# Kernel optimization log

Measured on AMD Instinct MI355X. Metric: run time of the kernel, lower is better.

## Reference

```python
import jax, jax.numpy as jnp
import numpy as np

L, H, E, V, BS = 12, 12, 768, 50257, 1024  # layers, heads, n_embd, vocab, block_size
B, T = 2, 1024
D = E // H


def setup_inputs() -> dict:
    key = jax.random.key(0)
    ks = jax.random.split(key, 10)
    s = 0.02
    d = {}
    d["idx"] = jax.random.randint(ks[0], (B, T), 0, V)
    d["targets"] = jax.random.randint(ks[1], (B, T), 0, V)
    # embeddings (wte tied with lm_head)
    d["wte"] = (jax.random.normal(ks[2], (V, E)) * s).astype(jnp.float32)
    d["wpe"] = (jax.random.normal(ks[3], (BS, E)) * s).astype(jnp.float32)
    # stacked per-layer params; Linear weights stored [in, out] (= torch W.T)
    d["ln1_w"] = jnp.ones((L, E), jnp.float32)
    d["ln1_b"] = jnp.zeros((L, E), jnp.float32)
    d["attn_w"] = (jax.random.normal(ks[4], (L, E, 3 * E)) * s).astype(jnp.float32)
    d["attn_b"] = jnp.zeros((L, 3 * E), jnp.float32)
    d["proj_w"] = (jax.random.normal(ks[5], (L, E, E)) * s).astype(jnp.float32)
    d["proj_b"] = jnp.zeros((L, E), jnp.float32)
    d["ln2_w"] = jnp.ones((L, E), jnp.float32)
    d["ln2_b"] = jnp.zeros((L, E), jnp.float32)
    d["fc_w"] = (jax.random.normal(ks[6], (L, E, 4 * E)) * s).astype(jnp.float32)
    d["fc_b"] = jnp.zeros((L, 4 * E), jnp.float32)
    d["fcproj_w"] = (jax.random.normal(ks[7], (L, 4 * E, E)) * s).astype(jnp.float32)
    d["fcproj_b"] = jnp.zeros((L, E), jnp.float32)
    d["lnf_w"] = jnp.ones((E,), jnp.float32)
    d["lnf_b"] = jnp.zeros((E,), jnp.float32)
    return d


def _ln(x, w, b, eps=1e-5):
    m = jnp.mean(x, -1, keepdims=True)
    v = jnp.mean(jnp.square(x - m), -1, keepdims=True)
    return (x - m) * jax.lax.rsqrt(v + eps) * w + b


def _block(x, p, mask):
    l1w, l1b, aw, ab, pw, pb, l2w, l2b, fw, fb, fpw, fpb = p
    Bx, Tx, C = x.shape
    # causal self-attention (explicit QK^T + mask + softmax + AV, as in source)
    qkv = _ln(x, l1w, l1b) @ aw + ab                       # [B,T,3E]
    q, k, v = jnp.split(qkv, 3, axis=-1)
    q = q.reshape(Bx, Tx, H, D).transpose(0, 2, 1, 3)       # [B,H,T,D]
    k = k.reshape(Bx, Tx, H, D).transpose(0, 2, 1, 3)
    v = v.reshape(Bx, Tx, H, D).transpose(0, 2, 1, 3)
    att = jnp.einsum('bhqd,bhkd->bhqk', q, k) * (1.0 / np.sqrt(D))
    att = jnp.where(mask, att, -jnp.inf)
    att = jax.nn.softmax(att, axis=-1)
    y = jnp.einsum('bhqk,bhkd->bhqd', att, v)
    y = y.transpose(0, 2, 1, 3).reshape(Bx, Tx, C)
    x = x + y @ pw + pb
    # MLP with tanh-approx GELU
    h = jax.nn.gelu(_ln(x, l2w, l2b) @ fw + fb, approximate=True)
    x = x + h @ fpw + fpb
    return x


def reference(idx, targets, wte, wpe, ln1_w, ln1_b, attn_w, attn_b, proj_w, proj_b,
              ln2_w, ln2_b, fc_w, fc_b, fcproj_w, fcproj_b, lnf_w, lnf_b):
    Tq = idx.shape[1]
    x = wte[idx] + wpe[:Tq]                                 # [B,T,E]
    mask = jnp.tril(jnp.ones((Tq, Tq), dtype=bool))

    def step(x, p):
        return _block(x, p, mask), None

    layer_params = (ln1_w, ln1_b, attn_w, attn_b, proj_w, proj_b,
                    ln2_w, ln2_b, fc_w, fc_b, fcproj_w, fcproj_b)
    x, _ = jax.lax.scan(step, x, layer_params)
    x = _ln(x, lnf_w, lnf_b)
    logits = x @ wte.T                                      # tied lm_head, [B,T,V]
    logp = jax.nn.log_softmax(logits, axis=-1)
    nll = -jnp.take_along_axis(logp, targets[..., None], axis=-1)[..., 0]
    loss = jnp.mean(nll)
    return logits, loss
```

## Files before the change

### kernel.cpp

```cpp
#include <hip/hip_runtime.h>
#include <hip/hip_bf16.h>
#include <math.h>

#define LNUM 12
#define HNUM 12
#define EDIM 768
#define VDIM 50257
#define BDIM 2
#define TDIM 1024
#define BT (BDIM*TDIM)
#define E3 (3*EDIM)
#define E4 (4*EDIM)
#define NPB (2*((VDIM+127)/128))

typedef __bf16 bf16x8 __attribute__((ext_vector_type(8)));
typedef __bf16 bf16x4 __attribute__((ext_vector_type(4)));
typedef float f32x4 __attribute__((ext_vector_type(4)));

__device__ __forceinline__ float gelu_f(float x) {
    float u = 0.7978845608028654f * (x + 0.044715f * x * x * x);
    return 0.5f * x * (1.0f + tanhf(u));
}

__device__ __forceinline__ void gl16(const void* g, void* l) {
    __builtin_amdgcn_global_load_lds(
        (const __attribute__((address_space(1))) unsigned int*)g,
        (__attribute__((address_space(3))) unsigned int*)l,
        16, 0, 0);
}

__global__ __launch_bounds__(256) void embed_kernel(
    const int* __restrict__ idx, const float* __restrict__ wte,
    const float* __restrict__ wpe, float* __restrict__ x)
{
    const int row = blockIdx.x;
    const int t = row % TDIM;
    const int tok = idx[row];
    const float* we = wte + (size_t)tok * EDIM;
    const float* pe = wpe + (size_t)t * EDIM;
    float* xr = x + (size_t)row * EDIM;
    for (int e = threadIdx.x; e < EDIM; e += 256) xr[e] = we[e] + pe[e];
}

__global__ __launch_bounds__(256) void ln_kernel(
    const float* __restrict__ in, const float* __restrict__ w,
    const float* __restrict__ b, __bf16* __restrict__ out)
{
    const int row = blockIdx.x * 4 + (threadIdx.x >> 6);
    const int lane = threadIdx.x & 63;
    const float4* xr = (const float4*)(in + (size_t)row * EDIM);
    float4 a0 = xr[lane], a1 = xr[64 + lane], a2 = xr[128 + lane];
    float s = a0.x + a0.y + a0.z + a0.w + a1.x + a1.y + a1.z + a1.w
            + a2.x + a2.y + a2.z + a2.w;
    #pragma unroll
    for (int off = 32; off; off >>= 1) s += __shfl_xor(s, off);
    const float mean = s * (1.0f / EDIM);
    float4 d0 = make_float4(a0.x - mean, a0.y - mean, a0.z - mean, a0.w - mean);
    float4 d1 = make_float4(a1.x - mean, a1.y - mean, a1.z - mean, a1.w - mean);
    float4 d2 = make_float4(a2.x - mean, a2.y - mean, a2.z - mean, a2.w - mean);
    float v = d0.x*d0.x + d0.y*d0.y + d0.z*d0.z + d0.w*d0.w
            + d1.x*d1.x + d1.y*d1.y + d1.z*d1.z + d1.w*d1.w
            + d2.x*d2.x + d2.y*d2.y + d2.z*d2.z + d2.w*d2.w;
    #pragma unroll
    for (int off = 32; off; off >>= 1) v += __shfl_xor(v, off);
    const float inv = rsqrtf(v * (1.0f / EDIM) + 1e-5f);
    const float4* w4 = (const float4*)w;
    const float4* b4 = (const float4*)b;
    __bf16* orow = out + (size_t)row * EDIM;
    #pragma unroll
    for (int c = 0; c < 3; ++c) {
        float4 dd = c == 0 ? d0 : (c == 1 ? d1 : d2);
        float4 ww = w4[c * 64 + lane], bb = b4[c * 64 + lane];
        bf16x4 o;
        o[0] = (__bf16)(dd.x * inv * ww.x + bb.x);
        o[1] = (__bf16)(dd.y * inv * ww.y + bb.y);
        o[2] = (__bf16)(dd.z * inv * ww.z + bb.z);
        o[3] = (__bf16)(dd.w * inv * ww.w + bb.w);
        *(bf16x4*)(orow + c * 256 + lane * 4) = o;
    }
}

__global__ __launch_bounds__(256) void redln_kernel(
    const float* __restrict__ ps, const float* __restrict__ bias,
    float* __restrict__ x, const float* __restrict__ w,
    const float* __restrict__ b, __bf16* __restrict__ out)
{
    const int row = blockIdx.x * 4 + (threadIdx.x >> 6);
    const int lane = threadIdx.x & 63;
    const float4* p0 = (const float4*)(ps + (size_t)row * EDIM);
    const float4* p1 = (const float4*)(ps + (size_t)(BT + row) * EDIM);
    float4* xr = (float4*)(x + (size_t)row * EDIM);
    const float4* b4 = (const float4*)bias;
    float4 a[3];
    #pragma unroll
    for (int c = 0; c < 3; ++c) {
        const int i = c * 64 + lane;
        float4 u = p0[i], v = p1[i], xx = xr[i], bb = b4[i];
        a[c] = make_float4(u.x + v.x + xx.x + bb.x, u.y + v.y + xx.y + bb.y,
                           u.z + v.z + xx.z + bb.z, u.w + v.w + xx.w + bb.w);
        xr[i] = a[c];
    }
    float s = a[0].x + a[0].y + a[0].z + a[0].w + a[1].x + a[1].y + a[1].z + a[1].w
            + a[2].x + a[2].y + a[2].z + a[2].w;
    #pragma unroll
    for (int off = 32; off; off >>= 1) s += __shfl_xor(s, off);
    const float mean = s * (1.0f / EDIM);
    float v = 0.f;
    #pragma unroll
    for (int c = 0; c < 3; ++c) {
        a[c] = make_float4(a[c].x - mean, a[c].y - mean, a[c].z - mean, a[c].w - mean);
        v += a[c].x * a[c].x + a[c].y * a[c].y + a[c].z * a[c].z + a[c].w * a[c].w;
    }
    #pragma unroll
    for (int off = 32; off; off >>= 1) v += __shfl_xor(v, off);
    const float inv = rsqrtf(v * (1.0f / EDIM) + 1e-5f);
    const float4* w4 = (const float4*)w;
    const float4* lb4 = (const float4*)b;
    __bf16* orow = out + (size_t)row * EDIM;
    #pragma unroll
    for (int c = 0; c < 3; ++c) {
        float4 ww = w4[c * 64 + lane], bb = lb4[c * 64 + lane];
        bf16x4 o;
        o[0] = (__bf16)(a[c].x * inv * ww.x + bb.x);
        o[1] = (__bf16)(a[c].y * inv * ww.y + bb.y);
        o[2] = (__bf16)(a[c].z * inv * ww.z + bb.z);
        o[3] = (__bf16)(a[c].w * inv * ww.w + bb.w);
        *(bf16x4*)(orow + c * 256 + lane * 4) = o;
    }
}

__global__ __launch_bounds__(256) void convt_kernel(
    const float* __restrict__ in, __bf16* __restrict__ out, int K, int N)
{
    in  += (size_t)blockIdx.z * K * N;
    out += (size_t)blockIdx.z * K * N;
    __shared__ float t[32][33];
    const int n0 = blockIdx.x * 32, k0 = blockIdx.y * 32;
    const int r = threadIdx.x >> 3, c = (threadIdx.x & 7) * 4;
    float4 v = *(const float4*)(in + (size_t)(k0 + r) * N + n0 + c);
    t[r][c + 0] = v.x; t[r][c + 1] = v.y; t[r][c + 2] = v.z; t[r][c + 3] = v.w;
    __syncthreads();
    bf16x4 o;
    o[0] = (__bf16)t[c + 0][r];
    o[1] = (__bf16)t[c + 1][r];
    o[2] = (__bf16)t[c + 2][r];
    o[3] = (__bf16)t[c + 3][r];
    *(bf16x4*)(out + (size_t)(n0 + r) * K + k0 + c) = o;
}

__global__ __launch_bounds__(256) void cvt_kernel(
    const float* __restrict__ in, __bf16* __restrict__ out, long n4)
{
    for (long i = blockIdx.x * 256L + threadIdx.x; i < n4; i += (long)gridDim.x * 256L) {
        float4 v = ((const float4*)in)[i];
        out[i * 4 + 0] = (__bf16)v.x;
        out[i * 4 + 1] = (__bf16)v.y;
        out[i * 4 + 2] = (__bf16)v.z;
        out[i * 4 + 3] = (__bf16)v.w;
    }
}

template<int BM, int BN, int BK, bool BIAS, bool GELU_, bool RES_, bool OUTBF, bool NGUARD>
__global__ __launch_bounds__(256, 2) void mgemm(
    const __bf16* __restrict__ A, const __bf16* __restrict__ Bt,
    const float* __restrict__ bias, const float* __restrict__ res,
    void* __restrict__ Cout, int M, int N, int K, int lda)
{
    constexpr int WM = BM / 2, WN = BN / 2;
    constexpr int FM = WM / 16, FN = WN / 16;
    constexpr int KS = BK / 32;
    constexpr int TBA = BM * BK * 2;
    constexpr int TBB = BN * BK * 2;
    constexpr int rA = TBA / 4096, rB = TBB / 4096;
    constexpr int RPI = 2048 / BK;
    constexpr int CPR = BK / 8;
    __shared__ __align__(16) __bf16 As[3 * BM * BK];
    __shared__ __align__(16) __bf16 Bs[3 * BN * BK];
    const int tid = threadIdx.x;
    const int lane = tid & 63;
    const int wave = tid >> 6;
    const int wr = wave >> 1, wc = wave & 1;

    const int bm = blockIdx.y, bn = blockIdx.x;
    const int m0 = bm * BM;
    const int n0 = bn * BN;
    const int kbase = blockIdx.z * K;
    const size_t zoff = (size_t)blockIdx.z * M * N;

    const int srow = tid / CPR;
    const int skey = (BK == 32) ? ((srow >> 1) & 3) : (srow & 7);
    const int c0 = (tid % CPR) ^ skey;

    const __bf16* gA = A + (size_t)(m0 + srow) * lda + kbase + c0 * 8;
    const __bf16* gB[rB];
    #pragma unroll
    for (int r = 0; r < rB; ++r) {
        int nr = n0 + srow + r * RPI;
        if (NGUARD) nr = nr < N ? nr : N - 1;
        gB[r] = Bt + (size_t)nr * lda + kbase + c0 * 8;
    }

    const int fr = lane & 15;
    const int g = lane >> 4;
    const int fkey = (BK == 32) ? ((fr >> 1) & 3) : (fr & 7);

    f32x4 acc[FM][FN];
    #pragma unroll
    for (int i = 0; i < FM; i++)
        #pragma unroll
        for (int j = 0; j < FN; j++) acc[i][j] = (f32x4){0.f, 0.f, 0.f, 0.f};

    const int nt = K / BK;

    auto stage = [&](int kk, int b) {
        #pragma unroll
        for (int r = 0; r < rA; ++r)
            gl16(gA + (size_t)r * RPI * lda + kk, (char*)As + b * TBA + r * 4096 + tid * 16);
        #pragma unroll
        for (int r = 0; r < rB; ++r)
            gl16(gB[r] + kk, (char*)Bs + b * TBB + r * 4096 + tid * 16);
    };

    stage(0, 0);
    if (nt > 1) stage(BK, 1);

    int b0 = 0, b1 = 1, b2 = 2;
    for (int t = 0; t < nt; ++t) {
        if (t + 1 < nt) {
            static_assert(rA + rB == 4 || rA + rB == 6, "vmcnt literal");
            if constexpr (rA + rB == 4) asm volatile("s_waitcnt vmcnt(4)" ::: "memory");
            else                        asm volatile("s_waitcnt vmcnt(6)" ::: "memory");
        } else {
            asm volatile("s_waitcnt vmcnt(0)" ::: "memory");
        }
        asm volatile("s_barrier" ::: "memory");
        if (t + 2 < nt) stage((t + 2) * BK, b2);

        const char* pa = (const char*)As + b0 * TBA;
        const char* pb = (const char*)Bs + b0 * TBB;
        bf16x8 af[FM][KS], bfr[FN][KS];
        #pragma unroll
        for (int i = 0; i < FM; i++)
            #pragma unroll
            for (int kc = 0; kc < KS; kc++)
                af[i][kc] = *(const bf16x8*)(pa + (wr * WM + i * 16 + fr) * (2 * BK)
                                                + (((kc * 4 + g) ^ fkey) << 4));
        #pragma unroll
        for (int j = 0; j < FN; j++)
            #pragma unroll
            for (int kc = 0; kc < KS; kc++)
                bfr[j][kc] = *(const bf16x8*)(pb + (wc * WN + j * 16 + fr) * (2 * BK)
                                                 + (((kc * 4 + g) ^ fkey) << 4));
        #pragma unroll
        for (int kc = 0; kc < KS; kc++)
            #pragma unroll
            for (int i = 0; i < FM; i++)
                #pragma unroll
                for (int j = 0; j < FN; j++)
                    acc[i][j] = __builtin_amdgcn_mfma_f32_16x16x32_bf16(af[i][kc], bfr[j][kc], acc[i][j], 0, 0, 0);
        const int tmp = b0; b0 = b1; b1 = b2; b2 = tmp;
    }

    const int crow = g * 4;
    #pragma unroll
    for (int i = 0; i < FM; i++) {
        #pragma unroll
        for (int r = 0; r < 4; r++) {
            const int m = m0 + wr * WM + i * 16 + crow + r;
            #pragma unroll
            for (int j = 0; j < FN; j++) {
                const int n = n0 + wc * WN + j * 16 + fr;
                if (!NGUARD || n < N) {
                    float v = acc[i][j][r];
                    if (BIAS) v += bias[n];
                    if (GELU_) v = gelu_f(v);
                    if (RES_) v += res[(size_t)m * N + n];
                    if (OUTBF) ((__bf16*)Cout)[zoff + (size_t)m * N + n] = (__bf16)v;
                    else       ((float*)Cout)[zoff + (size_t)m * N + n] = v;
                }
            }
        }
    }
}

__global__ __launch_bounds__(512, 1) void lgemm(
    const __bf16* __restrict__ A, const __bf16* __restrict__ Bt,
    float* __restrict__ Cout, float* __restrict__ part, int M, int N, int K)
{
    __shared__ __align__(16) __bf16 As[3 * 256 * 64];
    __shared__ __align__(16) __bf16 Bs[3 * 128 * 64];
    const int tid = threadIdx.x;
    const int lane = tid & 63;
    const int wave = tid >> 6;
    const int wm = wave >> 1, wn = wave & 1;

    const int wg = blockIdx.x;
    const int bm = (wg >> 3) & 7;
    const int bn = (wg & 7) + ((wg >> 6) << 3);
    if (bn * 128 >= N) return;
    const int m0 = bm * 256, n0 = bn * 128;

    const int srow = tid >> 3;
    const int c0 = (tid & 7) ^ (srow & 7);
    const __bf16* gA = A + (size_t)(m0 + srow) * K + c0 * 8;
    const __bf16* gB[2];
    #pragma unroll
    for (int r = 0; r < 2; ++r) {
        int nr = n0 + r * 64 + srow;
        nr = nr < N ? nr : N - 1;
        gB[r] = Bt + (size_t)nr * K + c0 * 8;
    }

    const int fr = lane & 15;
    const int g = lane >> 4;
    const int fk = fr & 7;

    auto stageA = [&](int kk, int b, int r) {
        gl16(gA + (size_t)r * 64 * K + kk, (char*)As + b * 32768 + r * 8192 + tid * 16);
    };
    auto stageB = [&](int kk, int b, int r) {
        gl16(gB[r] + kk, (char*)Bs + b * 16384 + r * 8192 + tid * 16);
    };

    f32x4 acc[4][4];
    #pragma unroll
    for (int i = 0; i < 4; i++)
        #pragma unroll
        for (int j = 0; j < 4; j++) acc[i][j] = (f32x4){0.f, 0.f, 0.f, 0.f};

    const int nt = K >> 6;
    #pragma unroll
    for (int r = 0; r < 4; ++r) stageA(0, 0, r);
    #pragma unroll
    for (int r = 0; r < 2; ++r) stageB(0, 0, r);
    #pragma unroll
    for (int r = 0; r < 4; ++r) stageA(64, 1, r);
    #pragma unroll
    for (int r = 0; r < 2; ++r) stageB(64, 1, r);

    for (int t = 0; t < nt; ++t) {
        const int bt = t % 3;
        if (t + 1 < nt) asm volatile("s_waitcnt vmcnt(6)" ::: "memory");
        else            asm volatile("s_waitcnt vmcnt(0)" ::: "memory");
        asm volatile("s_barrier" ::: "memory");

        const char* pa = (const char*)As + bt * 32768;
        const char* pb = (const char*)Bs + bt * 16384;
        const int kk2 = (t + 2) * 64;
        const int b2 = (t + 2) % 3;

        bf16x8 bfr[4][2], af[2][2];
        #pragma unroll
        for (int j = 0; j < 4; ++j)
            #pragma unroll
            for (int kc = 0; kc < 2; ++kc)
                bfr[j][kc] = *(const bf16x8*)(pb + (wn * 64 + j * 16 + fr) * 128
                                                 + (((kc * 4 + g) ^ fk) << 4));
        #pragma unroll
        for (int i = 0; i < 2; ++i)
            #pragma unroll
            for (int kc = 0; kc < 2; ++kc)
                af[i][kc] = *(const bf16x8*)(pa + (wm * 64 + i * 16 + fr) * 128
                                                + (((kc * 4 + g) ^ fk) << 4));
        if (t + 2 < nt) { stageA(kk2, b2, 0); stageA(kk2, b2, 1); stageA(kk2, b2, 2); }
        __builtin_amdgcn_s_setprio(1);
        #pragma unroll
        for (int kc = 0; kc < 2; ++kc)
            #pragma unroll
            for (int i = 0; i < 2; ++i)
                #pragma unroll
                for (int j = 0; j < 4; ++j)
                    acc[i][j] = __builtin_amdgcn_mfma_f32_16x16x32_bf16(af[i][kc], bfr[j][kc], acc[i][j], 0, 0, 0);
        __builtin_amdgcn_s_setprio(0);

        bf16x8 af1[2][2];
        #pragma unroll
        for (int i = 0; i < 2; ++i)
            #pragma unroll
            for (int kc = 0; kc < 2; ++kc)
                af1[i][kc] = *(const bf16x8*)(pa + (wm * 64 + (i + 2) * 16 + fr) * 128
                                                 + (((kc * 4 + g) ^ fk) << 4));
        if (t + 2 < nt) { stageA(kk2, b2, 3); stageB(kk2, b2, 0); stageB(kk2, b2, 1); }
        __builtin_amdgcn_s_setprio(1);
        #pragma unroll
        for (int kc = 0; kc < 2; ++kc)
            #pragma unroll
            for (int i = 0; i < 2; ++i)
                #pragma unroll
                for (int j = 0; j < 4; ++j)
                    acc[i + 2][j] = __builtin_amdgcn_mfma_f32_16x16x32_bf16(af1[i][kc], bfr[j][kc], acc[i + 2][j], 0, 0, 0);
        __builtin_amdgcn_s_setprio(0);
    }

    const int crow = g * 4;
    const int cg = bn * 2 + wn;
    #pragma unroll
    for (int i = 0; i < 4; i++) {
        #pragma unroll
        for (int r = 0; r < 4; r++) {
            const int m = m0 + wm * 64 + i * 16 + crow + r;
            float se = 0.f;
            #pragma unroll
            for (int j = 0; j < 4; j++) {
                const int n = n0 + wn * 64 + j * 16 + fr;
                if (n < N) {
                    float v = acc[i][j][r];
                    __builtin_nontemporal_store(v, &Cout[(size_t)m * N + n]);
                    se += __expf(v);
                }
            }
            se += __shfl_xor(se, 1); se += __shfl_xor(se, 2);
            se += __shfl_xor(se, 4); se += __shfl_xor(se, 8);
            if (fr == 0 && (n0 + wn * 64) < N)
                part[(size_t)m * NPB + cg] = se;
        }
    }
}

__global__ __launch_bounds__(128) void fattn_kernel(
    const __bf16* __restrict__ qkv, __bf16* __restrict__ y)
{
    const int bq = gridDim.x - 1 - blockIdx.x;
    const int h = blockIdx.y, b = blockIdx.z;
    const int tid = threadIdx.x, lane = tid & 63, w = tid >> 6;
    const int fr = lane & 15, g = lane >> 4;

    __shared__ __align__(16) __bf16 Ks[64 * 64];
    __shared__ __align__(16) __bf16 Vt[64 * 64];
    __shared__ __align__(16) __bf16 Ps[2][16 * 64];

    const __bf16* base = qkv + (size_t)b * TDIM * E3;
    const int q0w = bq * 32 + w * 16;
    const int NT = (bq >> 1) + 1;
    const int last = NT - 1;

    bf16x8 qf[2];
    {
        const __bf16* qp = base + (size_t)(q0w + fr) * E3 + h * 64 + g * 8;
        qf[0] = *(const bf16x8*)qp;
        qf[1] = *(const bf16x8*)(qp + 32);
        const __bf16 sc = (__bf16)0.125f;
        #pragma unroll
        for (int e = 0; e < 8; ++e) { qf[0][e] *= sc; qf[1][e] *= sc; }
    }

    const int r0 = tid >> 3, ch = tid & 7;
    bf16x8 kr[4], vr[4];

    #pragma unroll
    for (int it = 0; it < 4; ++it) {
        const int row = it * 16 + r0;
        const __bf16* gp = base + (size_t)row * E3 + EDIM + h * 64 + ch * 8;
        kr[it] = *(const bf16x8*)gp;
        vr[it] = *(const bf16x8*)(gp + EDIM);
    }
    #pragma unroll
    for (int it = 0; it < 4; ++it) {
        const int row = it * 16 + r0;
        *(bf16x8*)(Ks + row * 64 + ((ch ^ (row & 7)) << 3)) = kr[it];
        #pragma unroll
        for (int j = 0; j < 8; ++j) {
            const int d = ch * 8 + j;
            const int key = ((d >> 3) ^ d) & 7;
            Vt[d * 64 + ((((row >> 3) ^ key) << 3) + (row & 7))] = vr[it][j];
        }
    }
    __syncthreads();

    float m[4] = {-1e30f, -1e30f, -1e30f, -1e30f};
    float l[4] = {0.f, 0.f, 0.f, 0.f};
    f32x4 acc[4];
    #pragma unroll
    for (int jd = 0; jd < 4; ++jd) acc[jd] = (f32x4){0.f, 0.f, 0.f, 0.f};

    for (int kt = 0; kt < NT; ++kt) {
        if (kt < last) {
            const int k1 = (kt + 1) * 64;
            #pragma unroll
            for (int it = 0; it < 4; ++it) {
                const int row = it * 16 + r0;
                const __bf16* gp = base + (size_t)(k1 + row) * E3 + EDIM + h * 64 + ch * 8;
                kr[it] = *(const bf16x8*)gp;
                vr[it] = *(const bf16x8*)(gp + EDIM);
            }
        }

        const int k0 = kt * 64;
        f32x4 s[4];
        __builtin_amdgcn_s_setprio(1);
        #pragma unroll
        for (int jf = 0; jf < 4; ++jf) {
            const int krow = jf * 16 + fr;
            f32x4 sv = (f32x4){0.f, 0.f, 0.f, 0.f};
            #pragma unroll
            for (int kc = 0; kc < 2; ++kc) {
                bf16x8 kf = *(const bf16x8*)(Ks + krow * 64 + (((kc * 4 + g) ^ (fr & 7)) << 3));
                sv = __builtin_amdgcn_mfma_f32_16x16x32_bf16(qf[kc], kf, sv, 0, 0, 0);
            }
            s[jf] = sv;
        }
        __builtin_amdgcn_s_setprio(0);
        if (kt == last) {
            #pragma unroll
            for (int jf = 0; jf < 4; ++jf) {
                const int k = k0 + jf * 16 + fr;
                #pragma unroll
                for (int r = 0; r < 4; ++r) {
                    const int q = q0w + g * 4 + r;
                    if (k > q) s[jf][r] = -1e30f;
                }
            }
        }

        #pragma unroll
        for (int r = 0; r < 4; ++r) {
            float mx = fmaxf(fmaxf(s[0][r], s[1][r]), fmaxf(s[2][r], s[3][r]));
            mx = fmaxf(mx, __shfl_xor(mx, 1));
            mx = fmaxf(mx, __shfl_xor(mx, 2));
            mx = fmaxf(mx, __shfl_xor(mx, 4));
            mx = fmaxf(mx, __shfl_xor(mx, 8));
            const float mn = fmaxf(m[r], mx);
            const float sc2 = __expf(m[r] - mn);
            m[r] = mn;
            float rs = 0.f;
            #pragma unroll
            for (int jf = 0; jf < 4; ++jf) {
                const float p = __expf(s[jf][r] - mn);
                s[jf][r] = p;
                rs += p;
            }
            rs += __shfl_xor(rs, 1);
            rs += __shfl_xor(rs, 2);
            rs += __shfl_xor(rs, 4);
            rs += __shfl_xor(rs, 8);
            l[r] = l[r] * sc2 + rs;
            #pragma unroll
            for (int jd = 0; jd < 4; ++jd) acc[jd][r] *= sc2;
        }

        __bf16* pw = &Ps[w][0];
        #pragma unroll
        for (int jf = 0; jf < 4; ++jf) {
            const int chp = jf * 2 + (fr >> 3);
            #pragma unroll
            for (int r = 0; r < 4; ++r) {
                const int row = g * 4 + r;
                pw[row * 64 + (((chp ^ (row & 7)) << 3) + (fr & 7))] = (__bf16)s[jf][r];
            }
        }
        asm volatile("s_waitcnt lgkmcnt(0)" ::: "memory");
        bf16x8 pa[2];
        #pragma unroll
        for (int kc = 0; kc < 2; ++kc)
            pa[kc] = *(const bf16x8*)(pw + fr * 64 + (((kc * 4 + g) ^ (fr & 7)) << 3));

        __builtin_amdgcn_s_setprio(1);
        #pragma unroll
        for (int jd = 0; jd < 4; ++jd) {
            const int d = jd * 16 + fr;
            const int key = ((d >> 3) ^ d) & 7;
            #pragma unroll
            for (int kc = 0; kc < 2; ++kc) {
                bf16x8 vf = *(const bf16x8*)(Vt + d * 64 + (((kc * 4 + g) ^ key) << 3));
                acc[jd] = __builtin_amdgcn_mfma_f32_16x16x32_bf16(pa[kc], vf, acc[jd], 0, 0, 0);
            }
        }
        __builtin_amdgcn_s_setprio(0);

        if (kt < last) {
            __syncthreads();
            #pragma unroll
            for (int it = 0; it < 4; ++it) {
                const int row = it * 16 + r0;
                *(bf16x8*)(Ks + row * 64 + ((ch ^ (row & 7)) << 3)) = kr[it];
                #pragma unroll
                for (int j = 0; j < 8; ++j) {
                    const int d = ch * 8 + j;
                    const int key = ((d >> 3) ^ d) & 7;
                    Vt[d * 64 + ((((row >> 3) ^ key) << 3) + (row & 7))] = vr[it][j];
                }
            }
            __syncthreads();
        }
    }

    #pragma unroll
    for (int r = 0; r < 4; ++r) {
        const float inv = 1.0f / l[r];
        const int q = q0w + g * 4 + r;
        __bf16* yp = y + ((size_t)(b * TDIM + q)) * EDIM + h * 64;
        #pragma unroll
        for (int jd = 0; jd < 4; ++jd)
            yp[jd * 16 + fr] = (__bf16)(acc[jd][r] * inv);
    }
}

__global__ __launch_bounds__(256) void lsefin_kernel(
    const float* __restrict__ part, const float* __restrict__ logits,
    const int* __restrict__ targets, float* __restrict__ rr)
{
    const int row = blockIdx.x, tid = threadIdx.x;
    float s = 0.f;
    for (int j = tid; j < NPB; j += 256) s += part[(size_t)row * NPB + j];
    #pragma unroll
    for (int off = 32; off; off >>= 1) s += __shfl_xor(s, off);
    __shared__ float red[4];
    if ((tid & 63) == 0) red[tid >> 6] = s;
    __syncthreads();
    if (tid == 0) {
        float S = red[0] + red[1] + red[2] + red[3];
        rr[row] = logf(S) - logits[(size_t)row * VDIM + targets[row]];
    }
}

__global__ __launch_bounds__(256) void loss_reduce_kernel(
    const float* __restrict__ rr, float* __restrict__ out)
{
    const int tid = threadIdx.x;
    float s = 0.f;
    for (int i = tid; i < BT; i += 256) s += rr[i];
    #pragma unroll
    for (int off = 32; off; off >>= 1) s += __shfl_xor(s, off);
    __shared__ float red[4];
    if ((tid & 63) == 0) red[tid >> 6] = s;
    __syncthreads();
    if (tid == 0) out[0] = (red[0] + red[1] + red[2] + red[3]) * (1.0f / BT);
}

extern "C" void kernel_launch(void* const* d_in, const int* in_sizes, int n_in,
                              void* d_out, int out_size, void* d_ws, size_t ws_size,
                              hipStream_t stream)
{
    const int*   idx     = (const int*)d_in[0];
    const int*   targets = (const int*)d_in[1];
    const float* wte     = (const float*)d_in[2];
    const float* wpe     = (const float*)d_in[3];
    const float* ln1_w   = (const float*)d_in[4];
    const float* ln1_b   = (const float*)d_in[5];
    const float* attn_w  = (const float*)d_in[6];
    const float* attn_b  = (const float*)d_in[7];
    const float* proj_w  = (const float*)d_in[8];
    const float* proj_b  = (const float*)d_in[9];
    const float* ln2_w   = (const float*)d_in[10];
    const float* ln2_b   = (const float*)d_in[11];
    const float* fc_w    = (const float*)d_in[12];
    const float* fc_b    = (const float*)d_in[13];
    const float* fcp_w   = (const float*)d_in[14];
    const float* fcp_b   = (const float*)d_in[15];
    const float* lnf_w   = (const float*)d_in[16];
    const float* lnf_b   = (const float*)d_in[17];

    float* logits = (float*)d_out;

    const size_t slq = (size_t)EDIM * E3, slp = (size_t)EDIM * EDIM;
    const size_t slf = (size_t)EDIM * E4, slfp = (size_t)E4 * EDIM;

    char* wp = (char*)d_ws;
    float*  x     = (float*)wp;   wp += (size_t)BT * EDIM * 4;
    __bf16* qkvb  = (__bf16*)wp;  wp += (size_t)BT * E3 * 2;
    __bf16* xnbf  = (__bf16*)wp;  wp += (size_t)BT * EDIM * 2;
    __bf16* ybf   = (__bf16*)wp;  wp += (size_t)BT * EDIM * 2;
    __bf16* hbf   = (__bf16*)wp;  wp += (size_t)BT * E4 * 2;
    __bf16* wteb  = (__bf16*)wp;  wp += (size_t)VDIM * EDIM * 2;
    float*  part  = (float*)wp;   wp += (size_t)BT * NPB * 4;
    float*  psum  = (float*)wp;   wp += (size_t)2 * BT * EDIM * 4;
    float*  rr    = (float*)wp;   wp += (size_t)BT * 4;
    __bf16* wqkvb = (__bf16*)wp;

    const size_t wbytes_all = (slq + slp + slf + slfp) * 2 * LNUM;
    const size_t used = (size_t)(wp - (char*)d_ws);
    const bool big = ws_size >= used + wbytes_all;
    const size_t L = big ? LNUM : 1;
    __bf16* wprjb = wqkvb + slq * L;
    __bf16* wfcb  = wprjb + slp * L;
    __bf16* wfpb  = wfcb  + slf * L;

    embed_kernel<<<BT, 256, 0, stream>>>(idx, wte, wpe, x);
    cvt_kernel<<<2048, 256, 0, stream>>>(wte, wteb, (long)VDIM * EDIM / 4);

    if (big) {
        convt_kernel<<<dim3(E3 / 32, EDIM / 32, LNUM), 256, 0, stream>>>(attn_w, wqkvb, EDIM, E3);
        convt_kernel<<<dim3(EDIM / 32, EDIM / 32, LNUM), 256, 0, stream>>>(proj_w, wprjb, EDIM, EDIM);
        convt_kernel<<<dim3(E4 / 32, EDIM / 32, LNUM), 256, 0, stream>>>(fc_w, wfcb, EDIM, E4);
        convt_kernel<<<dim3(EDIM / 32, E4 / 32, LNUM), 256, 0, stream>>>(fcp_w, wfpb, E4, EDIM);
    }

    ln_kernel<<<BT / 4, 256, 0, stream>>>(x, ln1_w, ln1_b, xnbf);

    for (int l = 0; l < LNUM; ++l) {
        const __bf16* wq = wqkvb + (big ? (size_t)l * slq : 0);
        const __bf16* wpj = wprjb + (big ? (size_t)l * slp : 0);
        const __bf16* wf = wfcb + (big ? (size_t)l * slf : 0);
        const __bf16* wfp = wfpb + (big ? (size_t)l * slfp : 0);

        if (!big)
            convt_kernel<<<dim3(E3 / 32, EDIM / 32), 256, 0, stream>>>(
                attn_w + (size_t)l * slq, (__bf16*)wq, EDIM, E3);
        mgemm<64, 64, 64, true, false, false, true, false>
            <<<dim3(E3 / 64, BT / 64), 256, 0, stream>>>(
            xnbf, wq, attn_b + (size_t)l * E3, nullptr, qkvb, BT, E3, EDIM, EDIM);
        fattn_kernel<<<dim3(TDIM / 32, HNUM, BDIM), 128, 0, stream>>>(qkvb, ybf);
        if (!big)
            convt_kernel<<<dim3(EDIM / 32, EDIM / 32), 256, 0, stream>>>(
                proj_w + (size_t)l * slp, (__bf16*)wpj, EDIM, EDIM);
        mgemm<64, 64, 64, false, false, false, false, false>
            <<<dim3(EDIM / 64, BT / 64, 2), 256, 0, stream>>>(
            ybf, wpj, nullptr, nullptr, psum, BT, EDIM, EDIM / 2, EDIM);
        redln_kernel<<<BT / 4, 256, 0, stream>>>(
            psum, proj_b + (size_t)l * EDIM, x,
            ln2_w + (size_t)l * EDIM, ln2_b + (size_t)l * EDIM, xnbf);
        if (!big)
            convt_kernel<<<dim3(E4 / 32, EDIM / 32), 256, 0, stream>>>(
                fc_w + (size_t)l * slf, (__bf16*)wf, EDIM, E4);
        mgemm<64, 64, 64, true, true, false, true, false>
            <<<dim3(E4 / 64, BT / 64), 256, 0, stream>>>(
            xnbf, wf, fc_b + (size_t)l * E4, nullptr, hbf, BT, E4, EDIM, EDIM);
        if (!big)
            convt_kernel<<<dim3(EDIM / 32, E4 / 32), 256, 0, stream>>>(
                fcp_w + (size_t)l * slfp, (__bf16*)wfp, E4, EDIM);
        mgemm<64, 64, 64, false, false, false, false, false>
            <<<dim3(EDIM / 64, BT / 64, 2), 256, 0, stream>>>(
            hbf, wfp, nullptr, nullptr, psum, BT, EDIM, E4 / 2, E4);
        const float* nw = (l + 1 < LNUM) ? ln1_w + (size_t)(l + 1) * EDIM : lnf_w;
        const float* nb = (l + 1 < LNUM) ? ln1_b + (size_t)(l + 1) * EDIM : lnf_b;
        redln_kernel<<<BT / 4, 256, 0, stream>>>(
            psum, fcp_b + (size_t)l * EDIM, x, nw, nb, xnbf);
    }

    lgemm<<<dim3(64 * 50), 512, 0, stream>>>(
        xnbf, wteb, logits, part, BT, VDIM, EDIM);
    lsefin_kernel<<<BT, 256, 0, stream>>>(part, logits, targets, rr);
    loss_reduce_kernel<<<1, 256, 0, stream>>>(rr, logits + (size_t)BT * VDIM);
}
```

Baseline: 2.028 ms.

## Deepen lm_head GEMM pipeline to six K=32 stages with issue-ahead of four

Restructures the LM-head GEMM's shared-memory pipeline. The K tile shrinks from 64 to 32 with six LDS buffers and loads issued four tiles ahead, using graded vmcnt waits and a new swizzle for 64-byte rows. It also drops the separate A/B half-step interleaving and replaces nontemporal logit stores with ordinary stores. The goal is to hide more global-memory latency, at the cost of twice as many barriers per K and a different cache policy for the large logits write.

New measurement: 2.087 ms. 1.03x slower.

```diff
diff --git a/kernel.cpp b/kernel.cpp
--- a/kernel.cpp
+++ b/kernel.cpp
@@ -287,8 +287,8 @@
     const __bf16* __restrict__ A, const __bf16* __restrict__ Bt,
     float* __restrict__ Cout, float* __restrict__ part, int M, int N, int K)
 {
-    __shared__ __align__(16) __bf16 As[3 * 256 * 64];
-    __shared__ __align__(16) __bf16 Bs[3 * 128 * 64];
+    __shared__ __align__(16) __bf16 As[6 * 256 * 32];
+    __shared__ __align__(16) __bf16 Bs[6 * 128 * 32];
     const int tid = threadIdx.x;
     const int lane = tid & 63;
     const int wave = tid >> 6;
@@ -300,27 +300,24 @@
     if (bn * 128 >= N) return;
     const int m0 = bm * 256, n0 = bn * 128;
 
-    const int srow = tid >> 3;
-    const int c0 = (tid & 7) ^ (srow & 7);
+    const int srow = tid >> 2;
+    const int c0 = (tid & 3) ^ ((srow >> 1) & 3);
     const __bf16* gA = A + (size_t)(m0 + srow) * K + c0 * 8;
-    const __bf16* gB[2];
-    #pragma unroll
-    for (int r = 0; r < 2; ++r) {
-        int nr = n0 + r * 64 + srow;
-        nr = nr < N ? nr : N - 1;
-        gB[r] = Bt + (size_t)nr * K + c0 * 8;
-    }
+    int nr = n0 + srow; nr = nr < N ? nr : N - 1;
+    const __bf16* gB = Bt + (size_t)nr * K + c0 * 8;
 
     const int fr = lane & 15;
     const int g = lane >> 4;
-    const int fk = fr & 7;
-
-    auto stageA = [&](int kk, int b, int r) {
-        gl16(gA + (size_t)r * 64 * K + kk, (char*)As + b * 32768 + r * 8192 + tid * 16);
+    const int fkey = (fr >> 1) & 3;
+    const int slot = ((g ^ fkey) << 4);
+
+    auto stage = [&](int t) {
+        const int kk = t << 5;
+        const int b = t % 6;
+        gl16(gA + kk,                   (char*)As + b * 16384 + tid * 16);
+        gl16(gA + (size_t)128 * K + kk, (char*)As + b * 16384 + 8192 + tid * 16);
+        gl16(gB + kk,                   (char*)Bs + b * 8192 + tid * 16);
     };
-    auto stageB = [&](int kk, int b, int r) {
-        gl16(gB[r] + kk, (char*)Bs + b * 16384 + r * 8192 + tid * 16);
-    };
 
     f32x4 acc[4][4];
     #pragma unroll
@@ -328,67 +325,32 @@
         #pragma unroll
         for (int j = 0; j < 4; j++) acc[i][j] = (f32x4){0.f, 0.f, 0.f, 0.f};
 
-    const int nt = K >> 6;
-    #pragma unroll
-    for (int r = 0; r < 4; ++r) stageA(0, 0, r);
-    #pragma unroll
-    for (int r = 0; r < 2; ++r) stageB(0, 0, r);
-    #pragma unroll
-    for (int r = 0; r < 4; ++r) stageA(64, 1, r);
-    #pragma unroll
-    for (int r = 0; r < 2; ++r) stageB(64, 1, r);
+    const int nt = K >> 5;
+    stage(0); stage(1); stage(2); stage(3);
 
     for (int t = 0; t < nt; ++t) {
-        const int bt = t % 3;
-        if (t + 1 < nt) asm volatile("s_waitcnt vmcnt(6)" ::: "memory");
-        else            asm volatile("s_waitcnt vmcnt(0)" ::: "memory");
+        if (t + 4 <= nt)      asm volatile("s_waitcnt vmcnt(9)" ::: "memory");
+        else if (t + 3 <= nt) asm volatile("s_waitcnt vmcnt(6)" ::: "memory");
+        else if (t + 2 <= nt) asm volatile("s_waitcnt vmcnt(3)" ::: "memory");
+        else                  asm volatile("s_waitcnt vmcnt(0)" ::: "memory");
         asm volatile("s_barrier" ::: "memory");
-
-        const char* pa = (const char*)As + bt * 32768;
-        const char* pb = (const char*)Bs + bt * 16384;
-        const int kk2 = (t + 2) * 64;
-        const int b2 = (t + 2) % 3;
-
-        bf16x8 bfr[4][2], af[2][2];
+        if (t + 4 < nt) stage(t + 4);
+
+        const char* pa = (const char*)As + (t % 6) * 16384;
+        const char* pb = (const char*)Bs + (t % 6) * 8192;
+        bf16x8 af[4], bfr[4];
+        #pragma unroll
+        for (int i = 0; i < 4; ++i)
+            af[i] = *(const bf16x8*)(pa + (wm * 64 + i * 16 + fr) * 64 + slot);
         #pragma unroll
         for (int j = 0; j < 4; ++j)
-            #pragma unroll
-            for (int kc = 0; kc < 2; ++kc)
-                bfr[j][kc] = *(const bf16x8*)(pb + (wn * 64 + j * 16 + fr) * 128
-                                                 + (((kc * 4 + g) ^ fk) << 4));
-        #pragma unroll
-        for (int i = 0; i < 2; ++i)
-            #pragma unroll
-            for (int kc = 0; kc < 2; ++kc)
-                af[i][kc] = *(const bf16x8*)(pa + (wm * 64 + i * 16 + fr) * 128
-                                                + (((kc * 4 + g) ^ fk) << 4));
-        if (t + 2 < nt) { stageA(kk2, b2, 0); stageA(kk2, b2, 1); stageA(kk2, b2, 2); }
+            bfr[j] = *(const bf16x8*)(pb + (wn * 64 + j * 16 + fr) * 64 + slot);
         __builtin_amdgcn_s_setprio(1);
         #pragma unroll
-        for (int kc = 0; kc < 2; ++kc)
-            #pragma unroll
-            for (int i = 0; i < 2; ++i)
-                #pragma unroll
-                for (int j = 0; j < 4; ++j)
-                    acc[i][j] = __builtin_amdgcn_mfma_f32_16x16x32_bf16(af[i][kc], bfr[j][kc], acc[i][j], 0, 0, 0);
-        __builtin_amdgcn_s_setprio(0);
-
-        bf16x8 af1[2][2];
-        #pragma unroll
-        for (int i = 0; i < 2; ++i)
-            #pragma unroll
-            for (int kc = 0; kc < 2; ++kc)
-                af1[i][kc] = *(const bf16x8*)(pa + (wm * 64 + (i + 2) * 16 + fr) * 128
-                                                 + (((kc * 4 + g) ^ fk) << 4));
-        if (t + 2 < nt) { stageA(kk2, b2, 3); stageB(kk2, b2, 0); stageB(kk2, b2, 1); }
-        __builtin_amdgcn_s_setprio(1);
-        #pragma unroll
-        for (int kc = 0; kc < 2; ++kc)
-            #pragma unroll
-            for (int i = 0; i < 2; ++i)
-                #pragma unroll
-                for (int j = 0; j < 4; ++j)
-                    acc[i + 2][j] = __builtin_amdgcn_mfma_f32_16x16x32_bf16(af1[i][kc], bfr[j][kc], acc[i + 2][j], 0, 0, 0);
+        for (int i = 0; i < 4; ++i)
+            #pragma unroll
+            for (int j = 0; j < 4; ++j)
+                acc[i][j] = __builtin_amdgcn_mfma_f32_16x16x32_bf16(af[i], bfr[j], acc[i][j], 0, 0, 0);
         __builtin_amdgcn_s_setprio(0);
     }
 
@@ -405,7 +367,7 @@
                 const int n = n0 + wn * 64 + j * 16 + fr;
                 if (n < N) {
                     float v = acc[i][j][r];
-                    __builtin_nontemporal_store(v, &Cout[(size_t)m * N + n]);
+                    Cout[(size_t)m * N + n] = v;
                     se += __expf(v);
                 }
             }
```
